# Kernel tuning notes

Hardware: AMD Instinct MI355X
Metric: run time of the kernel (lower is better)

## Reference

```python
import jax, jax.numpy as jnp
import numpy as np
from jax import lax

EPS = 1e-5


def _feature_map(t):
    # squared-ReLU feature map + L2 normalize over channel dim (torch F.normalize dim=1)
    t = jax.nn.relu(t) + EPS
    t = t * t
    n = jnp.sqrt(jnp.sum(t * t, axis=1, keepdims=True))
    return t / jnp.maximum(n, 1e-12)


def _forward(x, qkv_w, qkv_b, dwc_w, dwc_b, norm_w, proj_w, proj_b):
    B, C, H, W = x.shape
    N = H * W
    d = norm_w.shape[0]
    # qkv: 1x1 conv (ConvNorm with BN folded into weight/bias)
    qkv = jnp.einsum('bchw,oc->bohw', x, qkv_w) + qkv_b[None, :, None, None]
    qkv = qkv.reshape(B, 3 * d, N)
    q, k, v = jnp.split(qkv, 3, axis=1)  # each [B, d, N]
    q = _feature_map(q)
    k = _feature_map(k)
    # linear-attention associativity path (N > d): attn = (v @ kT) @ q / z
    scale = N ** (-0.5)  # kT.shape[-2] == N
    kmean = jnp.mean(k, axis=2)                       # kT.mean(-2) -> [B, d]
    z = jnp.einsum('bd,bdn->bn', kmean, q)[:, None, :] + EPS  # [B,1,N]
    vkT = jnp.einsum('bin,bjn->bij', v * scale, k * scale)    # [B,d,d]
    attn = jnp.einsum('bij,bjn->bin', vkT, q) / z             # [B,d,N]
    # attn_norm: RMSNorm over channel dim with learnable per-channel weight
    rms = jnp.sqrt(jnp.mean(attn * attn, axis=1, keepdims=True) + EPS)
    attn = attn / rms * norm_w[None, :, None]
    attn = attn.reshape(B, d, H, W)
    # depthwise conv branch on v (RepConv folded to single depthwise conv)
    v_img = v.reshape(B, d, H, W)
    dw = lax.conv_general_dilated(
        v_img, dwc_w, window_strides=(1, 1), padding='SAME',
        feature_group_count=d,
        dimension_numbers=('NCHW', 'OIHW', 'NCHW'))
    dw = dw + dwc_b[None, :, None, None]
    y = attn + dw
    # proj: 1x1 conv d -> dim
    return jnp.einsum('bdhw,cd->bchw', y, proj_w) + proj_b[None, :, None, None]


def setup_inputs() -> dict:
    key = jax.random.key(0)
    ks = jax.random.split(key, 5)
    B, C, H, W = 16, 256, 64, 64
    d, kk = 256, 5
    x = jax.random.normal(ks[0], (B, C, H, W), jnp.float32)
    qkv_w = jax.random.normal(ks[1], (3 * d, C), jnp.float32) * 0.02
    qkv_b = jnp.zeros((3 * d,), jnp.float32)
    dwc_w = jax.random.normal(ks[2], (d, 1, kk, kk), jnp.float32) * 0.02
    dwc_b = jnp.zeros((d,), jnp.float32)
    norm_w = jnp.ones((d,), jnp.float32)
    proj_w = jax.random.normal(ks[3], (C, d), jnp.float32) * 0.02
    proj_b = jnp.zeros((C,), jnp.float32)
    return {'x': x, 'qkv_w': qkv_w, 'qkv_b': qkv_b, 'dwc_w': dwc_w,
            'dwc_b': dwc_b, 'norm_w': norm_w, 'proj_w': proj_w, 'proj_b': proj_b}


def reference(x, qkv_w, qkv_b, dwc_w, dwc_b, norm_w, proj_w, proj_b):
    return _forward(x, qkv_w, qkv_b, dwc_w, dwc_b, norm_w, proj_w, proj_b)
```

## Files before the change

kernel.cpp:

```cpp
#include <hip/hip_runtime.h>
#include <math.h>
#include <stdint.h>

#define FLA_EPS 1e-5f

constexpr int kB  = 16;
constexpr int kD  = 256;
constexpr int kN  = 4096;
constexpr int kO3 = 768;

typedef __attribute__((ext_vector_type(8))) short bf16x8;
typedef __attribute__((ext_vector_type(4))) float f32x4;

__device__ __forceinline__ unsigned short f2bf(float f) {
  union { float f; uint32_t u; } v; v.f = f;
  uint32_t r = v.u + 0x7FFFu + ((v.u >> 16) & 1u);
  return (unsigned short)(r >> 16);
}
__device__ __forceinline__ float bf2f(unsigned short h) {
  union { uint32_t u; float f; } v; v.u = ((uint32_t)h) << 16; return v.f;
}
__device__ __forceinline__ void gl_lds16(const void* g, void* l) {
  __builtin_amdgcn_global_load_lds(
      (const __attribute__((address_space(1))) uint32_t*)g,
      (__attribute__((address_space(3))) uint32_t*)l, 16, 0, 0);
}

__global__ __launch_bounds__(256) void convert_w(
    const float* __restrict__ w, unsigned short* __restrict__ wb, int n) {
  const int i = blockIdx.x * 256 + threadIdx.x;
  if (i < n) wb[i] = f2bf(w[i]);
}

__global__ __launch_bounds__(256) void transpose_x2(
    const float* __restrict__ x, unsigned short* __restrict__ xt) {
  __shared__ float t[64][65];
  const int tid = threadIdx.x;
  const int n0 = blockIdx.x * 64, c0 = blockIdx.y * 64, b = blockIdx.z;
  const float* xb = x + ((long)b * kD + c0) * kN + n0;
#pragma unroll
  for (int r = 0; r < 4; ++r) {
    const int idx = tid + r * 256;
    const int c = idx >> 4, n4 = (idx & 15) * 4;
    const float4 v = *(const float4*)(xb + (long)c * kN + n4);
    t[c][n4] = v.x; t[c][n4 + 1] = v.y; t[c][n4 + 2] = v.z; t[c][n4 + 3] = v.w;
  }
  __syncthreads();
  unsigned short* xtb = xt + ((long)b * kN + n0) * kD + c0;
#pragma unroll
  for (int r = 0; r < 4; ++r) {
    const int idx = tid + r * 256;
    const int n = idx >> 4, cg = (idx & 15) * 4;
    ushort4 o;
    o.x = f2bf(t[cg + 0][n]); o.y = f2bf(t[cg + 1][n]);
    o.z = f2bf(t[cg + 2][n]); o.w = f2bf(t[cg + 3][n]);
    *(ushort4*)&xtb[(long)n * kD + cg] = o;
  }
}

__global__ __launch_bounds__(256) void qkv7_mfma(
    const unsigned short* __restrict__ Wb, const unsigned short* __restrict__ xt,
    const float* __restrict__ bias, unsigned short* __restrict__ qt,
    unsigned short* __restrict__ kb, unsigned short* __restrict__ vb,
    float* __restrict__ km) {
  __shared__ unsigned short sA[256 * 32] __attribute__((aligned(16)));
  __shared__ unsigned short sB[64 * 32] __attribute__((aligned(16)));
  __shared__ float sBias[256];
  __shared__ float colbuf[4][64];
  const int tid = threadIdx.x;
  const int n0 = blockIdx.x * 64, type = blockIdx.y, b = blockIdx.z;
  const int m0 = type * 256;
  const unsigned short* xtb = xt + (long)b * kN * kD;
  const int lane = tid & 63, w = tid >> 6;
  const int lr = lane & 15, lq = lane >> 4;
  sBias[tid] = bias[m0 + tid];

  f32x4 acc[4][4];
#pragma unroll
  for (int i = 0; i < 4; ++i)
#pragma unroll
    for (int j = 0; j < 4; ++j) acc[i][j] = (f32x4){0.f, 0.f, 0.f, 0.f};

  for (int k0 = 0; k0 < 256; k0 += 32) {
#pragma unroll
    for (int r = 0; r < 4; ++r) {
      const int c = tid + r * 256;
      gl_lds16(Wb + (long)(m0 + (c >> 2)) * 256 + k0 + (c & 3) * 8, &sA[c * 8]);
    }
    {
      const int c = tid;
      gl_lds16(xtb + (long)(n0 + (c >> 2)) * kD + k0 + (c & 3) * 8, &sB[c * 8]);
    }
    __syncthreads();
    bf16x8 af[4], bfr[4];
#pragma unroll
    for (int mt = 0; mt < 4; ++mt)
      af[mt] = *(const bf16x8*)&sA[(w * 64 + mt * 16 + lr) * 32 + lq * 8];
#pragma unroll
    for (int nt = 0; nt < 4; ++nt)
      bfr[nt] = *(const bf16x8*)&sB[(nt * 16 + lr) * 32 + lq * 8];
#pragma unroll
    for (int mt = 0; mt < 4; ++mt)
#pragma unroll
      for (int nt = 0; nt < 4; ++nt)
        acc[mt][nt] = __builtin_amdgcn_mfma_f32_16x16x32_bf16(
            af[mt], bfr[nt], acc[mt][nt], 0, 0, 0);
    __syncthreads();
  }

  if (type < 2) {
    float part[4] = {0.f, 0.f, 0.f, 0.f};
#pragma unroll
    for (int mt = 0; mt < 4; ++mt) {
#pragma unroll
      for (int rr = 0; rr < 4; ++rr) {
        const float bv = sBias[w * 64 + mt * 16 + lq * 4 + rr];
#pragma unroll
        for (int nt = 0; nt < 4; ++nt) {
          const float r_ = fmaxf(acc[mt][nt][rr] + bv, 0.f) + FLA_EPS;
          const float t = r_ * r_;
          acc[mt][nt][rr] = t;
          part[nt] += t * t;
        }
      }
    }
#pragma unroll
    for (int nt = 0; nt < 4; ++nt) {
      part[nt] += __shfl_xor(part[nt], 16);
      part[nt] += __shfl_xor(part[nt], 32);
    }
    if (lq == 0)
#pragma unroll
      for (int nt = 0; nt < 4; ++nt) colbuf[w][nt * 16 + lr] = part[nt];
    __syncthreads();
    float inv[4];
#pragma unroll
    for (int nt = 0; nt < 4; ++nt) {
      const int col = nt * 16 + lr;
      const float S = colbuf[0][col] + colbuf[1][col] + colbuf[2][col] + colbuf[3][col];
      inv[nt] = 1.f / fmaxf(sqrtf(S), 1e-12f);
    }
    if (type == 0) {
      unsigned short* qtb = qt + (long)b * kN * kD;
#pragma unroll
      for (int mt = 0; mt < 4; ++mt)
#pragma unroll
        for (int nt = 0; nt < 4; ++nt) {
          ushort4 o;
          o.x = f2bf(acc[mt][nt][0] * inv[nt]);
          o.y = f2bf(acc[mt][nt][1] * inv[nt]);
          o.z = f2bf(acc[mt][nt][2] * inv[nt]);
          o.w = f2bf(acc[mt][nt][3] * inv[nt]);
          *(ushort4*)&qtb[(long)(n0 + nt * 16 + lr) * kD + w * 64 + mt * 16 + lq * 4] = o;
        }
    } else {
      unsigned short* kbb = kb + (long)b * kD * kN;
#pragma unroll
      for (int mt = 0; mt < 4; ++mt)
#pragma unroll
        for (int rr = 0; rr < 4; ++rr) {
          const int ch = w * 64 + mt * 16 + lq * 4 + rr;
          float ks = 0.f;
#pragma unroll
          for (int nt = 0; nt < 4; ++nt) {
            const unsigned short sv = f2bf(acc[mt][nt][rr] * inv[nt]);
            kbb[(long)ch * kN + n0 + nt * 16 + lr] = sv;
            ks += bf2f(sv);
          }
          ks += __shfl_xor(ks, 1);
          ks += __shfl_xor(ks, 2);
          ks += __shfl_xor(ks, 4);
          ks += __shfl_xor(ks, 8);
          if (lr == 0) atomicAdd(&km[b * kD + ch], ks * (1.f / kN));
        }
    }
  } else {
    unsigned short* vbb = vb + (long)b * kD * kN;
#pragma unroll
    for (int mt = 0; mt < 4; ++mt)
#pragma unroll
      for (int rr = 0; rr < 4; ++rr) {
        const int ch = w * 64 + mt * 16 + lq * 4 + rr;
        const float bv = sBias[ch];
#pragma unroll
        for (int nt = 0; nt < 4; ++nt)
          vbb[(long)ch * kN + n0 + nt * 16 + lr] = f2bf(acc[mt][nt][rr] + bv);
      }
  }
}

__global__ __launch_bounds__(256) void vkt2_mfma(
    const unsigned short* __restrict__ vb, const unsigned short* __restrict__ kb,
    float* __restrict__ Tpart) {
  __shared__ unsigned short sA[128 * 32] __attribute__((aligned(16)));
  __shared__ unsigned short sB[128 * 32] __attribute__((aligned(16)));
  const int tid = threadIdx.x;
  const int i0 = blockIdx.x * 128, j0 = blockIdx.y * 128;
  const int b = blockIdx.z >> 3, s = blockIdx.z & 7;
  const unsigned short* vbb = vb + (long)b * kD * kN;
  const unsigned short* kbb = kb + (long)b * kD * kN;
  const int lane = tid & 63, w = tid >> 6;
  const int wm = (w & 1) * 64, wn = (w >> 1) * 64;
  const int lr = lane & 15, lq = lane >> 4;
  const int c0 = tid, c1 = 256 + tid;
  const int am0 = c0 >> 2, ak0 = (c0 & 3) * 8;
  const int am1 = c1 >> 2, ak1 = (c1 & 3) * 8;

  f32x4 acc[4][4];
#pragma unroll
  for (int i = 0; i < 4; ++i)
#pragma unroll
    for (int j = 0; j < 4; ++j) acc[i][j] = (f32x4){0.f, 0.f, 0.f, 0.f};

  for (int n0 = s * 512; n0 < s * 512 + 512; n0 += 32) {
    gl_lds16(vbb + (long)(i0 + am0) * kN + n0 + ak0, &sA[c0 * 8]);
    gl_lds16(vbb + (long)(i0 + am1) * kN + n0 + ak1, &sA[c1 * 8]);
    gl_lds16(kbb + (long)(j0 + am0) * kN + n0 + ak0, &sB[c0 * 8]);
    gl_lds16(kbb + (long)(j0 + am1) * kN + n0 + ak1, &sB[c1 * 8]);
    __syncthreads();
    bf16x8 af[4], bf[4];
#pragma unroll
    for (int mt = 0; mt < 4; ++mt)
      af[mt] = *(const bf16x8*)&sA[(wm + mt * 16 + lr) * 32 + lq * 8];
#pragma unroll
    for (int nt = 0; nt < 4; ++nt)
      bf[nt] = *(const bf16x8*)&sB[(wn + nt * 16 + lr) * 32 + lq * 8];
#pragma unroll
    for (int mt = 0; mt < 4; ++mt)
#pragma unroll
      for (int nt = 0; nt < 4; ++nt)
        acc[mt][nt] = __builtin_amdgcn_mfma_f32_16x16x32_bf16(
            af[mt], bf[nt], acc[mt][nt], 0, 0, 0);
    __syncthreads();
  }
  float* Tp = Tpart + ((long)s * kB + b) * kD * kD;
#pragma unroll
  for (int mt = 0; mt < 4; ++mt)
#pragma unroll
    for (int nt = 0; nt < 4; ++nt) {
      const int j = j0 + wn + nt * 16 + lr;
#pragma unroll
      for (int r = 0; r < 4; ++r) {
        const int i = i0 + wm + mt * 16 + lq * 4 + r;
        Tp[(long)i * kD + j] = acc[mt][nt][r];
      }
    }
}

__global__ __launch_bounds__(256) void tconvert(
    const float* __restrict__ Tpart, unsigned short* __restrict__ Tt) {
  const long idx = (long)blockIdx.x * 256 + threadIdx.x;
  float s = 0.f;
#pragma unroll
  for (int p = 0; p < 8; ++p) s += Tpart[(long)p * 1048576 + idx];
  Tt[idx] = f2bf(s * (1.f / 4096.f));
}

__global__ __launch_bounds__(256) void dwconv3(
    const unsigned short* __restrict__ vb, const float* __restrict__ dwc_w,
    const float* __restrict__ dwc_b, unsigned short* __restrict__ dwp) {
  __shared__ float tile[68][80];
  __shared__ float wt[32];
  const int c = blockIdx.x, b = blockIdx.y;
  const int tid = threadIdx.x;
  if (tid < 25) wt[tid] = dwc_w[c * 25 + tid];
  {
    const float4 z4 = {0.f, 0.f, 0.f, 0.f};
    float* tf = &tile[0][0];
#pragma unroll
    for (int r = 0; r < 6; ++r) {
      const int i = tid + r * 256;
      if (i < 1360) *(float4*)(tf + i * 4) = z4;
    }
  }
  __syncthreads();
  const unsigned short* vp = vb + ((long)b * kD + c) * kN;
#pragma unroll
  for (int r = 0; r < 2; ++r) {
    const int ch = tid + r * 256;
    const int row = ch >> 3, sub = ch & 7;
    const uint4 u = *(const uint4*)(vp + row * 64 + sub * 8);
    const unsigned short* p = (const unsigned short*)&u;
    float4 f0, f1;
    f0.x = bf2f(p[0]); f0.y = bf2f(p[1]); f0.z = bf2f(p[2]); f0.w = bf2f(p[3]);
    f1.x = bf2f(p[4]); f1.y = bf2f(p[5]); f1.z = bf2f(p[6]); f1.w = bf2f(p[7]);
    *(float4*)&tile[row + 2][4 + sub * 8] = f0;
    *(float4*)&tile[row + 2][8 + sub * 8] = f1;
  }
  __syncthreads();
  float w_[25];
#pragma unroll
  for (int i = 0; i < 25; ++i) w_[i] = wt[i];
  const float bias = dwc_b[c];
  const int pr = tid >> 4, pc = tid & 15;
  const int oy0 = pr * 4, ox0 = pc * 4;
  float win[8][12];
#pragma unroll
  for (int r = 0; r < 8; ++r) {
    *(float4*)&win[r][0] = *(const float4*)&tile[oy0 + r][ox0 + 0];
    *(float4*)&win[r][4] = *(const float4*)&tile[oy0 + r][ox0 + 4];
    *(float4*)&win[r][8] = *(const float4*)&tile[oy0 + r][ox0 + 8];
  }
  unsigned short* yp = dwp + ((long)b * kD + c) * kN;
#pragma unroll
  for (int dy = 0; dy < 4; ++dy) {
    ushort4 o;
    unsigned short* op = (unsigned short*)&o;
#pragma unroll
    for (int dx = 0; dx < 4; ++dx) {
      float s = bias;
#pragma unroll
      for (int ky = 0; ky < 5; ++ky)
#pragma unroll
        for (int kx = 0; kx < 5; ++kx)
          s += win[dy + ky][dx + kx + 2] * w_[ky * 5 + kx];
      op[dx] = f2bf(s);
    }
    *(ushort4*)&yp[(oy0 + dy) * 64 + ox0] = o;
  }
}

__global__ __launch_bounds__(256) void attnproj_mfma(
    const unsigned short* __restrict__ qt, const unsigned short* __restrict__ Tt,
    const float* __restrict__ kmean, const float* __restrict__ norm_w,
    const unsigned short* __restrict__ dwp, const unsigned short* __restrict__ Pw,
    const float* __restrict__ proj_b, float* __restrict__ out) {
  __shared__ unsigned char smem[36864] __attribute__((aligned(16)));
  __shared__ unsigned short sY[64 * 264] __attribute__((aligned(16)));
  __shared__ float sKm[256];
  __shared__ float sNw[256];
  __shared__ float zbuf[64];
  __shared__ float rbuf[4][64];
  unsigned short* sQ = (unsigned short*)smem;
  unsigned short* sT = (unsigned short*)(smem + 4096);
  unsigned short* sDw = (unsigned short*)smem;
  unsigned short* sP = (unsigned short*)smem;
  const int tid = threadIdx.x;
  const int n0 = blockIdx.x * 64, b = blockIdx.y;
  const unsigned short* qtb = qt + (long)b * kN * kD;
  const unsigned short* Ttb = Tt + (long)b * kD * kD;
  sKm[tid] = kmean[b * kD + tid];
  sNw[tid] = norm_w[tid];
  const int lane = tid & 63, w = tid >> 6;
  const int lr = lane & 15, lq = lane >> 4;

  f32x4 acc[4][4];
#pragma unroll
  for (int i = 0; i < 4; ++i)
#pragma unroll
    for (int j = 0; j < 4; ++j) acc[i][j] = (f32x4){0.f, 0.f, 0.f, 0.f};
  float zp[4] = {0.f, 0.f, 0.f, 0.f};

  for (int k0 = 0; k0 < 256; k0 += 32) {
    {
      const int c = tid;
      gl_lds16(qtb + (long)(n0 + (c >> 2)) * kD + k0 + (c & 3) * 8, &sQ[c * 8]);
    }
#pragma unroll
    for (int r = 0; r < 4; ++r) {
      const int c = tid + r * 256;
      gl_lds16(Ttb + (long)(c >> 2) * kD + k0 + (c & 3) * 8, &sT[c * 8]);
    }
    __syncthreads();
    bf16x8 af[4], bf[4];
#pragma unroll
    for (int mt = 0; mt < 4; ++mt)
      af[mt] = *(const bf16x8*)&sQ[(mt * 16 + lr) * 32 + lq * 8];
#pragma unroll
    for (int nt = 0; nt < 4; ++nt)
      bf[nt] = *(const bf16x8*)&sT[(w * 64 + nt * 16 + lr) * 32 + lq * 8];
#pragma unroll
    for (int mt = 0; mt < 4; ++mt)
#pragma unroll
      for (int j = 0; j < 8; ++j)
        zp[mt] += bf2f((unsigned short)af[mt][j]) * sKm[k0 + lq * 8 + j];
#pragma unroll
    for (int mt = 0; mt < 4; ++mt)
#pragma unroll
      for (int nt = 0; nt < 4; ++nt)
        acc[mt][nt] = __builtin_amdgcn_mfma_f32_16x16x32_bf16(
            af[mt], bf[nt], acc[mt][nt], 0, 0, 0);
    __syncthreads();
  }

  const unsigned short* dwpb = dwp + (long)b * kD * kN;
#pragma unroll
  for (int it = 0; it < 8; ++it) {
    const int c = tid + it * 256;
    const int row = c >> 3, sub = c & 7;
    uint4 t4 = *(const uint4*)(dwpb + (long)row * kN + n0 + sub * 8);
    *(uint4*)&sDw[row * 72 + sub * 8] = t4;
  }
#pragma unroll
  for (int mt = 0; mt < 4; ++mt) {
    zp[mt] += __shfl_xor(zp[mt], 16);
    zp[mt] += __shfl_xor(zp[mt], 32);
  }
  if (w == 0 && lq == 0)
#pragma unroll
    for (int mt = 0; mt < 4; ++mt) zbuf[mt * 16 + lr] = zp[mt];
  __syncthreads();

  float ss[4][4];
#pragma unroll
  for (int mt = 0; mt < 4; ++mt)
#pragma unroll
    for (int r = 0; r < 4; ++r) {
      const float invz = 1.f / (zbuf[mt * 16 + lq * 4 + r] + FLA_EPS);
      float s = 0.f;
#pragma unroll
      for (int nt = 0; nt < 4; ++nt) {
        acc[mt][nt][r] *= invz;
        s += acc[mt][nt][r] * acc[mt][nt][r];
      }
      ss[mt][r] = s;
    }
#pragma unroll
  for (int mt = 0; mt < 4; ++mt)
#pragma unroll
    for (int r = 0; r < 4; ++r) {
      ss[mt][r] += __shfl_xor(ss[mt][r], 1);
      ss[mt][r] += __shfl_xor(ss[mt][r], 2);
      ss[mt][r] += __shfl_xor(ss[mt][r], 4);
      ss[mt][r] += __shfl_xor(ss[mt][r], 8);
    }
  if (lr == 0)
#pragma unroll
    for (int mt = 0; mt < 4; ++mt)
#pragma unroll
      for (int r = 0; r < 4; ++r) rbuf[w][mt * 16 + lq * 4 + r] = ss[mt][r];
  __syncthreads();

  float nw[4];
#pragma unroll
  for (int nt = 0; nt < 4; ++nt) nw[nt] = sNw[w * 64 + nt * 16 + lr];
#pragma unroll
  for (int mt = 0; mt < 4; ++mt)
#pragma unroll
    for (int r = 0; r < 4; ++r) {
      const int p = mt * 16 + lq * 4 + r;
      const float S = rbuf[0][p] + rbuf[1][p] + rbuf[2][p] + rbuf[3][p];
      const float scl = rsqrtf(S * (1.f / 256.f) + FLA_EPS);
#pragma unroll
      for (int nt = 0; nt < 4; ++nt) {
        const int ch = w * 64 + nt * 16 + lr;
        const float dw = bf2f(sDw[ch * 72 + p]);
        sY[p * 264 + ch] = f2bf(acc[mt][nt][r] * scl * nw[nt] + dw);
      }
    }
  __syncthreads();

  f32x4 acc2[4][4];
#pragma unroll
  for (int i = 0; i < 4; ++i)
#pragma unroll
    for (int j = 0; j < 4; ++j) acc2[i][j] = (f32x4){0.f, 0.f, 0.f, 0.f};
  int bo[4];
#pragma unroll
  for (int nt = 0; nt < 4; ++nt) bo[nt] = (nt * 16 + lr) * 264 + lq * 8;

  for (int kk = 0; kk < 8; ++kk) {
#pragma unroll
    for (int r = 0; r < 4; ++r) {
      const int c = tid + r * 256;
      gl_lds16(Pw + (long)(c >> 2) * 256 + kk * 32 + (c & 3) * 8, &sP[c * 8]);
    }
    __syncthreads();
    bf16x8 af[4], bf[4];
#pragma unroll
    for (int mt = 0; mt < 4; ++mt)
      af[mt] = *(const bf16x8*)&sP[(w * 64 + mt * 16 + lr) * 32 + lq * 8];
#pragma unroll
    for (int nt = 0; nt < 4; ++nt)
      bf[nt] = *(const bf16x8*)&sY[bo[nt] + kk * 32];
#pragma unroll
    for (int mt = 0; mt < 4; ++mt)
#pragma unroll
      for (int nt = 0; nt < 4; ++nt)
        acc2[mt][nt] = __builtin_amdgcn_mfma_f32_16x16x32_bf16(
            af[mt], bf[nt], acc2[mt][nt], 0, 0, 0);
    __syncthreads();
  }

  float* ob = out + (long)b * kD * kN;
#pragma unroll
  for (int mt = 0; mt < 4; ++mt)
#pragma unroll
    for (int r = 0; r < 4; ++r) {
      const int m = w * 64 + mt * 16 + lq * 4 + r;
      const float pb = proj_b[m];
#pragma unroll
      for (int nt = 0; nt < 4; ++nt)
        ob[(long)m * kN + n0 + nt * 16 + lr] = acc2[mt][nt][r] + pb;
    }
}

extern "C" void kernel_launch(void* const* d_in, const int* in_sizes, int n_in,
                              void* d_out, int out_size, void* d_ws,
                              size_t ws_size, hipStream_t stream) {
  const float* x      = (const float*)d_in[0];
  const float* qkv_w  = (const float*)d_in[1];
  const float* qkv_b  = (const float*)d_in[2];
  const float* dwc_w  = (const float*)d_in[3];
  const float* dwc_b  = (const float*)d_in[4];
  const float* norm_w = (const float*)d_in[5];
  const float* proj_w = (const float*)d_in[6];
  const float* proj_b = (const float*)d_in[7];
  float* out = (float*)d_out;
  char* ws = (char*)d_ws;

  constexpr long SZ = 33554432;
  unsigned short* qt  = (unsigned short*)(ws);
  unsigned short* kb  = (unsigned short*)(ws + SZ);
  unsigned short* vb  = (unsigned short*)(ws + 2 * SZ);
  unsigned short* dwp = (unsigned short*)(ws + 3 * SZ);
  unsigned short* xt  = (unsigned short*)(ws + 5 * SZ);
  float* Tpart        = (float*)(ws + 5 * SZ);
  unsigned short* Tt  = (unsigned short*)(ws + 6 * SZ);
  unsigned short* wqb = (unsigned short*)(ws + 6 * SZ + 2097152);
  unsigned short* wpb = (unsigned short*)(ws + 6 * SZ + 2097152 + 393216);
  float* km           = (float*)(ws + 6 * SZ + 2097152 + 393216 + 131072);

  convert_w<<<768, 256, 0, stream>>>(qkv_w, wqb, kO3 * kD);
  convert_w<<<256, 256, 0, stream>>>(proj_w, wpb, kD * kD);
  transpose_x2<<<dim3(64, 4, 16), 256, 0, stream>>>(x, xt);
  hipMemsetAsync(km, 0, kB * kD * sizeof(float), stream);
  qkv7_mfma<<<dim3(64, 3, 16), 256, 0, stream>>>(wqb, xt, qkv_b, qt, kb, vb, km);
  vkt2_mfma<<<dim3(2, 2, 128), 256, 0, stream>>>(vb, kb, Tpart);
  tconvert<<<4096, 256, 0, stream>>>(Tpart, Tt);
  dwconv3<<<dim3(256, 16), 256, 0, stream>>>(vb, dwc_w, dwc_b, dwp);
  attnproj_mfma<<<dim3(64, 16), 256, 0, stream>>>(qt, Tt, km, norm_w, dwp,
                                                  wpb, proj_b, out);
}
```

Measured before the change: 294.5 us.

## Double-buffer LDS tiles in GEMM kernels and compute key mean separately

The qkv, vkT and attention/projection GEMM loops now use two LDS buffers. The next K-slice is fetched with global-to-LDS loads while MFMAs run on the current slice, which removes one barrier per iteration and overlaps global latency with compute. The atomic per-channel key-mean accumulation in the qkv epilogue is replaced by a separate reduction kernel over the stored bf16 keys, and the memset goes away. The trade is a larger LDS footprint and an extra pass that reads the whole k tensor again.

```diff
diff --git a/kernel.cpp b/kernel.cpp
--- a/kernel.cpp
+++ b/kernel.cpp
@@ -58,13 +58,12 @@
   }
 }
 
-__global__ __launch_bounds__(256) void qkv7_mfma(
+__global__ __launch_bounds__(256) void qkv8_mfma(
     const unsigned short* __restrict__ Wb, const unsigned short* __restrict__ xt,
     const float* __restrict__ bias, unsigned short* __restrict__ qt,
-    unsigned short* __restrict__ kb, unsigned short* __restrict__ vb,
-    float* __restrict__ km) {
-  __shared__ unsigned short sA[256 * 32] __attribute__((aligned(16)));
-  __shared__ unsigned short sB[64 * 32] __attribute__((aligned(16)));
+    unsigned short* __restrict__ kb, unsigned short* __restrict__ vb) {
+  __shared__ unsigned short sA[2][256 * 32] __attribute__((aligned(16)));
+  __shared__ unsigned short sB[2][64 * 32] __attribute__((aligned(16)));
   __shared__ float sBias[256];
   __shared__ float colbuf[4][64];
   const int tid = threadIdx.x;
@@ -81,24 +80,40 @@
 #pragma unroll
     for (int j = 0; j < 4; ++j) acc[i][j] = (f32x4){0.f, 0.f, 0.f, 0.f};
 
-  for (int k0 = 0; k0 < 256; k0 += 32) {
-#pragma unroll
-    for (int r = 0; r < 4; ++r) {
-      const int c = tid + r * 256;
-      gl_lds16(Wb + (long)(m0 + (c >> 2)) * 256 + k0 + (c & 3) * 8, &sA[c * 8]);
-    }
-    {
-      const int c = tid;
-      gl_lds16(xtb + (long)(n0 + (c >> 2)) * kD + k0 + (c & 3) * 8, &sB[c * 8]);
-    }
-    __syncthreads();
+#pragma unroll
+  for (int r = 0; r < 4; ++r) {
+    const int c = tid + r * 256;
+    gl_lds16(Wb + (long)(m0 + (c >> 2)) * 256 + (c & 3) * 8, &sA[0][c * 8]);
+  }
+  {
+    const int c = tid;
+    gl_lds16(xtb + (long)(n0 + (c >> 2)) * kD + (c & 3) * 8, &sB[0][c * 8]);
+  }
+  __syncthreads();
+
+  for (int kk = 0; kk < 8; ++kk) {
+    const int cur = kk & 1;
+    if (kk < 7) {
+      const int k0 = (kk + 1) * 32;
+#pragma unroll
+      for (int r = 0; r < 4; ++r) {
+        const int c = tid + r * 256;
+        gl_lds16(Wb + (long)(m0 + (c >> 2)) * 256 + k0 + (c & 3) * 8,
+                 &sA[cur ^ 1][c * 8]);
+      }
+      {
+        const int c = tid;
+        gl_lds16(xtb + (long)(n0 + (c >> 2)) * kD + k0 + (c & 3) * 8,
+                 &sB[cur ^ 1][c * 8]);
+      }
+    }
     bf16x8 af[4], bfr[4];
 #pragma unroll
     for (int mt = 0; mt < 4; ++mt)
-      af[mt] = *(const bf16x8*)&sA[(w * 64 + mt * 16 + lr) * 32 + lq * 8];
+      af[mt] = *(const bf16x8*)&sA[cur][(w * 64 + mt * 16 + lr) * 32 + lq * 8];
 #pragma unroll
     for (int nt = 0; nt < 4; ++nt)
-      bfr[nt] = *(const bf16x8*)&sB[(nt * 16 + lr) * 32 + lq * 8];
+      bfr[nt] = *(const bf16x8*)&sB[cur][(nt * 16 + lr) * 32 + lq * 8];
 #pragma unroll
     for (int mt = 0; mt < 4; ++mt)
 #pragma unroll
@@ -160,18 +175,9 @@
 #pragma unroll
         for (int rr = 0; rr < 4; ++rr) {
           const int ch = w * 64 + mt * 16 + lq * 4 + rr;
-          float ks = 0.f;
-#pragma unroll
-          for (int nt = 0; nt < 4; ++nt) {
-            const unsigned short sv = f2bf(acc[mt][nt][rr] * inv[nt]);
-            kbb[(long)ch * kN + n0 + nt * 16 + lr] = sv;
-            ks += bf2f(sv);
-          }
-          ks += __shfl_xor(ks, 1);
-          ks += __shfl_xor(ks, 2);
-          ks += __shfl_xor(ks, 4);
-          ks += __shfl_xor(ks, 8);
-          if (lr == 0) atomicAdd(&km[b * kD + ch], ks * (1.f / kN));
+#pragma unroll
+          for (int nt = 0; nt < 4; ++nt)
+            kbb[(long)ch * kN + n0 + nt * 16 + lr] = f2bf(acc[mt][nt][rr] * inv[nt]);
         }
     }
   } else {
@@ -189,11 +195,33 @@
   }
 }
 
-__global__ __launch_bounds__(256) void vkt2_mfma(
+__global__ __launch_bounds__(256) void kmean2(
+    const unsigned short* __restrict__ kb, float* __restrict__ km) {
+  const int c = blockIdx.x, b = blockIdx.y;
+  const unsigned short* row = kb + ((long)b * kD + c) * kN;
+  const int base = threadIdx.x * 16;
+  float s = 0.f;
+#pragma unroll
+  for (int h = 0; h < 2; ++h) {
+    uint4 u = *(const uint4*)(row + base + h * 8);
+    const unsigned short* p = (const unsigned short*)&u;
+#pragma unroll
+    for (int i = 0; i < 8; ++i) s += bf2f(p[i]);
+  }
+#pragma unroll
+  for (int m = 1; m < 64; m <<= 1) s += __shfl_xor(s, m);
+  __shared__ float red[4];
+  if ((threadIdx.x & 63) == 0) red[threadIdx.x >> 6] = s;
+  __syncthreads();
+  if (threadIdx.x == 0)
+    km[b * kD + c] = (red[0] + red[1] + red[2] + red[3]) * (1.f / kN);
+}
+
+__global__ __launch_bounds__(256) void vkt5_mfma(
     const unsigned short* __restrict__ vb, const unsigned short* __restrict__ kb,
     float* __restrict__ Tpart) {
-  __shared__ unsigned short sA[128 * 32] __attribute__((aligned(16)));
-  __shared__ unsigned short sB[128 * 32] __attribute__((aligned(16)));
+  __shared__ unsigned short sA[2][128 * 32] __attribute__((aligned(16)));
+  __shared__ unsigned short sB[2][128 * 32] __attribute__((aligned(16)));
   const int tid = threadIdx.x;
   const int i0 = blockIdx.x * 128, j0 = blockIdx.y * 128;
   const int b = blockIdx.z >> 3, s = blockIdx.z & 7;
@@ -212,19 +240,29 @@
 #pragma unroll
     for (int j = 0; j < 4; ++j) acc[i][j] = (f32x4){0.f, 0.f, 0.f, 0.f};
 
-  for (int n0 = s * 512; n0 < s * 512 + 512; n0 += 32) {
-    gl_lds16(vbb + (long)(i0 + am0) * kN + n0 + ak0, &sA[c0 * 8]);
-    gl_lds16(vbb + (long)(i0 + am1) * kN + n0 + ak1, &sA[c1 * 8]);
-    gl_lds16(kbb + (long)(j0 + am0) * kN + n0 + ak0, &sB[c0 * 8]);
-    gl_lds16(kbb + (long)(j0 + am1) * kN + n0 + ak1, &sB[c1 * 8]);
-    __syncthreads();
+  const int nbase = s * 512;
+  gl_lds16(vbb + (long)(i0 + am0) * kN + nbase + ak0, &sA[0][c0 * 8]);
+  gl_lds16(vbb + (long)(i0 + am1) * kN + nbase + ak1, &sA[0][c1 * 8]);
+  gl_lds16(kbb + (long)(j0 + am0) * kN + nbase + ak0, &sB[0][c0 * 8]);
+  gl_lds16(kbb + (long)(j0 + am1) * kN + nbase + ak1, &sB[0][c1 * 8]);
+  __syncthreads();
+
+  for (int kk = 0; kk < 16; ++kk) {
+    const int cur = kk & 1;
+    if (kk < 15) {
+      const int n0 = nbase + (kk + 1) * 32;
+      gl_lds16(vbb + (long)(i0 + am0) * kN + n0 + ak0, &sA[cur ^ 1][c0 * 8]);
+      gl_lds16(vbb + (long)(i0 + am1) * kN + n0 + ak1, &sA[cur ^ 1][c1 * 8]);
+      gl_lds16(kbb + (long)(j0 + am0) * kN + n0 + ak0, &sB[cur ^ 1][c0 * 8]);
+      gl_lds16(kbb + (long)(j0 + am1) * kN + n0 + ak1, &sB[cur ^ 1][c1 * 8]);
+    }
     bf16x8 af[4], bf[4];
 #pragma unroll
     for (int mt = 0; mt < 4; ++mt)
-      af[mt] = *(const bf16x8*)&sA[(wm + mt * 16 + lr) * 32 + lq * 8];
+      af[mt] = *(const bf16x8*)&sA[cur][(wm + mt * 16 + lr) * 32 + lq * 8];
 #pragma unroll
     for (int nt = 0; nt < 4; ++nt)
-      bf[nt] = *(const bf16x8*)&sB[(wn + nt * 16 + lr) * 32 + lq * 8];
+      bf[nt] = *(const bf16x8*)&sB[cur][(wn + nt * 16 + lr) * 32 + lq * 8];
 #pragma unroll
     for (int mt = 0; mt < 4; ++mt)
 #pragma unroll
@@ -320,21 +358,18 @@
   }
 }
 
-__global__ __launch_bounds__(256) void attnproj_mfma(
+__global__ __launch_bounds__(256) void attnproj2_mfma(
     const unsigned short* __restrict__ qt, const unsigned short* __restrict__ Tt,
     const float* __restrict__ kmean, const float* __restrict__ norm_w,
     const unsigned short* __restrict__ dwp, const unsigned short* __restrict__ Pw,
     const float* __restrict__ proj_b, float* __restrict__ out) {
-  __shared__ unsigned char smem[36864] __attribute__((aligned(16)));
+  __shared__ unsigned char smem[40960] __attribute__((aligned(16)));
   __shared__ unsigned short sY[64 * 264] __attribute__((aligned(16)));
   __shared__ float sKm[256];
   __shared__ float sNw[256];
   __shared__ float zbuf[64];
   __shared__ float rbuf[4][64];
-  unsigned short* sQ = (unsigned short*)smem;
-  unsigned short* sT = (unsigned short*)(smem + 4096);
   unsigned short* sDw = (unsigned short*)smem;
-  unsigned short* sP = (unsigned short*)smem;
   const int tid = threadIdx.x;
   const int n0 = blockIdx.x * 64, b = blockIdx.y;
   const unsigned short* qtb = qt + (long)b * kN * kD;
@@ -351,17 +386,39 @@
     for (int j = 0; j < 4; ++j) acc[i][j] = (f32x4){0.f, 0.f, 0.f, 0.f};
   float zp[4] = {0.f, 0.f, 0.f, 0.f};
 
-  for (int k0 = 0; k0 < 256; k0 += 32) {
+  {
+    unsigned short* sQ = (unsigned short*)smem;
+    unsigned short* sT = (unsigned short*)(smem + 4096);
     {
       const int c = tid;
-      gl_lds16(qtb + (long)(n0 + (c >> 2)) * kD + k0 + (c & 3) * 8, &sQ[c * 8]);
+      gl_lds16(qtb + (long)(n0 + (c >> 2)) * kD + (c & 3) * 8, &sQ[c * 8]);
     }
 #pragma unroll
     for (int r = 0; r < 4; ++r) {
       const int c = tid + r * 256;
-      gl_lds16(Ttb + (long)(c >> 2) * kD + k0 + (c & 3) * 8, &sT[c * 8]);
-    }
-    __syncthreads();
+      gl_lds16(Ttb + (long)(c >> 2) * kD + (c & 3) * 8, &sT[c * 8]);
+    }
+  }
+  __syncthreads();
+
+  for (int kk = 0; kk < 8; ++kk) {
+    const int cur = kk & 1;
+    unsigned short* sQ = (unsigned short*)(smem + cur * 20480);
+    unsigned short* sT = (unsigned short*)(smem + cur * 20480 + 4096);
+    if (kk < 7) {
+      const int k0 = (kk + 1) * 32;
+      unsigned short* nQ = (unsigned short*)(smem + (cur ^ 1) * 20480);
+      unsigned short* nT = (unsigned short*)(smem + (cur ^ 1) * 20480 + 4096);
+      {
+        const int c = tid;
+        gl_lds16(qtb + (long)(n0 + (c >> 2)) * kD + k0 + (c & 3) * 8, &nQ[c * 8]);
+      }
+#pragma unroll
+      for (int r = 0; r < 4; ++r) {
+        const int c = tid + r * 256;
+        gl_lds16(Ttb + (long)(c >> 2) * kD + k0 + (c & 3) * 8, &nT[c * 8]);
+      }
+    }
     bf16x8 af[4], bf[4];
 #pragma unroll
     for (int mt = 0; mt < 4; ++mt)
@@ -373,7 +430,7 @@
     for (int mt = 0; mt < 4; ++mt)
 #pragma unroll
       for (int j = 0; j < 8; ++j)
-        zp[mt] += bf2f((unsigned short)af[mt][j]) * sKm[k0 + lq * 8 + j];
+        zp[mt] += bf2f((unsigned short)af[mt][j]) * sKm[kk * 32 + lq * 8 + j];
 #pragma unroll
     for (int mt = 0; mt < 4; ++mt)
 #pragma unroll
@@ -459,13 +516,28 @@
 #pragma unroll
   for (int nt = 0; nt < 4; ++nt) bo[nt] = (nt * 16 + lr) * 264 + lq * 8;
 
-  for (int kk = 0; kk < 8; ++kk) {
+  {
+    unsigned short* sP = (unsigned short*)smem;
 #pragma unroll
     for (int r = 0; r < 4; ++r) {
       const int c = tid + r * 256;
-      gl_lds16(Pw + (long)(c >> 2) * 256 + kk * 32 + (c & 3) * 8, &sP[c * 8]);
-    }
-    __syncthreads();
+      gl_lds16(Pw + (long)(c >> 2) * 256 + (c & 3) * 8, &sP[c * 8]);
+    }
+  }
+  __syncthreads();
+
+  for (int kk = 0; kk < 8; ++kk) {
+    const int cur = kk & 1;
+    unsigned short* sP = (unsigned short*)(smem + cur * 16384);
+    if (kk < 7) {
+      unsigned short* nP = (unsigned short*)(smem + (cur ^ 1) * 16384);
+#pragma unroll
+      for (int r = 0; r < 4; ++r) {
+        const int c = tid + r * 256;
+        gl_lds16(Pw + (long)(c >> 2) * 256 + (kk + 1) * 32 + (c & 3) * 8,
+                 &nP[c * 8]);
+      }
+    }
     bf16x8 af[4], bf[4];
 #pragma unroll
     for (int mt = 0; mt < 4; ++mt)
@@ -524,11 +596,11 @@
   convert_w<<<768, 256, 0, stream>>>(qkv_w, wqb, kO3 * kD);
   convert_w<<<256, 256, 0, stream>>>(proj_w, wpb, kD * kD);
   transpose_x2<<<dim3(64, 4, 16), 256, 0, stream>>>(x, xt);
-  hipMemsetAsync(km, 0, kB * kD * sizeof(float), stream);
-  qkv7_mfma<<<dim3(64, 3, 16), 256, 0, stream>>>(wqb, xt, qkv_b, qt, kb, vb, km);
-  vkt2_mfma<<<dim3(2, 2, 128), 256, 0, stream>>>(vb, kb, Tpart);
+  qkv8_mfma<<<dim3(64, 3, 16), 256, 0, stream>>>(wqb, xt, qkv_b, qt, kb, vb);
+  kmean2<<<dim3(256, 16), 256, 0, stream>>>(kb, km);
+  vkt5_mfma<<<dim3(2, 2, 128), 256, 0, stream>>>(vb, kb, Tpart);
   tconvert<<<4096, 256, 0, stream>>>(Tpart, Tt);
   dwconv3<<<dim3(256, 16), 256, 0, stream>>>(vb, dwc_w, dwc_b, dwp);
-  attnproj_mfma<<<dim3(64, 16), 256, 0, stream>>>(qt, Tt, km, norm_w, dwp,
-                                                  wpb, proj_b, out);
-}
+  attnproj2_mfma<<<dim3(64, 16), 256, 0, stream>>>(qt, Tt, km, norm_w, dwp,
+                                                   wpb, proj_b, out);
+}
```

After: 285.9 us. -2.9%, faster.
